# Optimization experiments

Measured on AMD Instinct MI355X. Metric: run time of the kernel, lower is better.

The kernel has to match this reference:

```python
import jax, jax.numpy as jnp
import numpy as np

NUM_CLUSTERS = 56
HEIGHT = 224
WIDTH = 224
BATCH = 32
FEAT_C = 64


def setup_inputs() -> dict:
    key = jax.random.key(0)
    combined_features = jax.random.normal(key, (BATCH, FEAT_C + 1, HEIGHT, WIDTH), dtype=jnp.float32)
    # std parameter init: num_clusters / sqrt(H*W)
    std = jnp.asarray(NUM_CLUSTERS / (HEIGHT * WIDTH) ** 0.5, dtype=jnp.float32)
    return {"combined_features": combined_features, "std": std}


def _sobel(edges):
    # edges: [B,1,H,W], 3x3 sobel with padding=1 (fixed, non-learnable filters)
    kx = jnp.array([[-1., 0., 1.], [-2., 0., 2.], [-1., 0., 1.]], jnp.float32)[None, None]
    ky = jnp.array([[-1., -2., -1.], [0., 0., 0.], [1., 2., 1.]], jnp.float32)[None, None]
    conv = lambda k: jax.lax.conv_general_dilated(edges, k, (1, 1), [(1, 1), (1, 1)])
    return conv(kx), conv(ky)


def reference(combined_features, std):
    B, Cp1, H, W = combined_features.shape
    K = NUM_CLUSTERS
    edges = combined_features[:, -1:]      # [B,1,H,W]
    features = combined_features[:, :-1]   # [B,C,H,W]

    # --- centroid seeding from edge map ---
    Gx, Gy = _sobel(edges)
    grad_mag = jnp.sqrt(Gx ** 2 + Gy ** 2)
    inverted = 1.0 - 0.5 * grad_mag                      # [B,1,H,W]
    # adaptive_avg_pool2d to (K,K); H,W divisible by K -> exact reshape-mean
    pooled = inverted[:, 0].reshape(B, K, H // K, K, W // K).mean(axis=(2, 4))  # [B,K,K]
    flat = pooled.reshape(B, K * K)
    _, idx = jax.lax.top_k(flat, K)                      # [B,K]
    sy = (idx // K).astype(jnp.float32) / K              # [B,K] in [0,1)
    sx = (idx % K).astype(jnp.float32) / K

    # --- spatial gaussian distance: separable over y and x ---
    y = (jnp.arange(H, dtype=jnp.float32) / H)[None, None, :, None]  # [1,1,H,1]
    x = (jnp.arange(W, dtype=jnp.float32) / W)[None, None, None, :]  # [1,1,1,W]
    dy = y - sy[:, :, None, None]                        # [B,K,H,1]
    dx = x - sx[:, :, None, None]                        # [B,K,1,W]
    # gauss2d(a,b,std) = (exp(-(a/std)^2) + exp(-(b/std)^2)) / 2
    spatial = (jnp.exp(-(dy / std) ** 2) + jnp.exp(-(dx / std) ** 2)) * 0.5  # [B,K,H,W]

    # --- feature distance of each pixel to global mean feature (eps=1e-6 as in F.pairwise_distance) ---
    centroid = features.mean(axis=(2, 3))                # [B,C]
    fdist = jnp.sqrt(jnp.sum((features - centroid[:, :, None, None] + 1e-6) ** 2, axis=1))  # [B,H,W]

    combined = spatial + fdist[:, None]                  # [B,K,H,W]
    markers = jax.nn.softmax(combined, axis=1)           # softmax over clusters
    return markers
```

## Files before the change

kernel.cpp:

```cpp
#include <hip/hip_runtime.h>
#include <math.h>

#define NCLUS 56
#define HH 224
#define WW 224
#define BB 32
#define CELLS (NCLUS * NCLUS)
#define HW (HH * WW)

typedef float f32x4 __attribute__((ext_vector_type(4)));

__global__ __launch_bounds__(256) void pool_kernel(const float* __restrict__ cf,
                                                   float* __restrict__ pooled) {
    __shared__ float lds[18][226];
    int b = blockIdx.x / 14;
    int grp = blockIdx.x - b * 14;
    int tid = threadIdx.x;
    const float* e = cf + ((size_t)b * 65 + 64) * HW;

    int y0 = grp * 16 - 1;
    for (int t = tid; t < 18 * 224; t += 256) {
        int r = t / 224;
        int c = t - r * 224;
        int y = y0 + r;
        lds[r][c + 1] = (y >= 0 && y < HH) ? e[y * WW + c] : 0.0f;
    }
    if (tid < 18) { lds[tid][0] = 0.0f; lds[tid][225] = 0.0f; }
    __syncthreads();

    if (tid >= 224) return;
    int lby = tid / 56;
    int bx = tid - lby * 56;
    int r0 = lby * 4;
    int c0 = bx * 4;

    float patch[6][6];
#pragma unroll
    for (int i = 0; i < 6; ++i)
#pragma unroll
        for (int j = 0; j < 6; ++j) patch[i][j] = lds[r0 + i][c0 + j];

    float s = 0.0f;
#pragma unroll
    for (int iy = 0; iy < 4; ++iy) {
#pragma unroll
        for (int ix = 0; ix < 4; ++ix) {
            float gx = (patch[iy][ix + 2] - patch[iy][ix])
                     + 2.0f * (patch[iy + 1][ix + 2] - patch[iy + 1][ix])
                     + (patch[iy + 2][ix + 2] - patch[iy + 2][ix]);
            float gy = (patch[iy + 2][ix] - patch[iy][ix])
                     + 2.0f * (patch[iy + 2][ix + 1] - patch[iy][ix + 1])
                     + (patch[iy + 2][ix + 2] - patch[iy][ix + 2]);
            float gm = sqrtf(gx * gx + gy * gy);
            s += 1.0f - 0.5f * gm;
        }
    }
    pooled[b * CELLS + (grp * 4 + lby) * NCLUS + bx] = s * 0.0625f;
}

__global__ __launch_bounds__(256) void topk_tables_kernel(
        const float* __restrict__ pooled, const float* __restrict__ stdp,
        float* __restrict__ Fx, float* __restrict__ Fy) {
    int b = blockIdx.x;
    int tid = threadIdx.x;
    __shared__ unsigned long long list[CELLS];
    __shared__ float sy_s[NCLUS], sx_s[NCLUS];
    __shared__ unsigned nlist_s;
    if (tid == 0) nlist_s = 0;

    if (tid < 64) {
        unsigned hi[49];
#pragma unroll
        for (int j = 0; j < 49; ++j) {
            int i = j * 64 + tid;
            unsigned u = __float_as_uint(pooled[b * CELLS + i]);
            hi[j] = (u & 0x80000000u) ? ~u : (u | 0x80000000u);
        }
        unsigned prefix = 0;
        unsigned cnt = CELLS;
        for (int bit = 31; bit >= 0; --bit) {
            if (cnt <= 448u) break;
            unsigned cand = prefix | (1u << bit);
            unsigned c = 0;
#pragma unroll
            for (int j = 0; j < 49; ++j) c += (hi[j] >= cand) ? 1u : 0u;
#pragma unroll
            for (int off = 32; off >= 1; off >>= 1)
                c += __shfl_xor(c, off, 64);
            if (c >= (unsigned)NCLUS) { prefix = cand; cnt = c; }
        }
#pragma unroll
        for (int j = 0; j < 49; ++j) {
            if (hi[j] >= prefix) {
                unsigned pos = atomicAdd(&nlist_s, 1u);
                unsigned i = (unsigned)(j * 64 + tid);
                list[pos] = ((unsigned long long)hi[j] << 32) |
                            (unsigned long long)(0xFFFFFFFFu - i);
            }
        }
    }
    __syncthreads();

    int N = (int)nlist_s;
    for (int c = tid; c < N; c += 256) {
        unsigned long long key = list[c];
        int r = 0;
        for (int j = 0; j < N; ++j) r += (list[j] > key) ? 1 : 0;
        if (r < NCLUS) {
            unsigned idx = 0xFFFFFFFFu - (unsigned)(key & 0xFFFFFFFFull);
            sy_s[r] = (float)(idx / NCLUS) / (float)NCLUS;
            sx_s[r] = (float)(idx % NCLUS) / (float)NCLUS;
        }
    }
    __syncthreads();

    float inv_std = 1.0f / stdp[0];
    for (int t = tid; t < NCLUS * WW; t += 256) {
        int k = t / WW;
        int w = t - k * WW;
        float tx = ((float)w / 224.0f - sx_s[k]) * inv_std;
        Fx[(size_t)b * NCLUS * WW + t] = expf(0.5f * expf(-(tx * tx)));
    }
    for (int t = tid; t < HH * NCLUS; t += 256) {
        int h = t / NCLUS;
        int k = t - h * NCLUS;
        float ty = ((float)h / 224.0f - sy_s[k]) * inv_std;
        Fy[(size_t)b * HH * NCLUS + t] = expf(0.5f * expf(-(ty * ty)));
    }
}

__global__ __launch_bounds__(448) void markers_kernel(
        const float* __restrict__ Fx, const float* __restrict__ Fy,
        float* __restrict__ out) {
    __shared__ float fx_lds[NCLUS][WW];
    __shared__ float fy_s[14 * NCLUS];
    int blk = blockIdx.x;
    int b = blk / 16;
    int h0 = (blk - b * 16) * 14;
    int tid = threadIdx.x;

    const f32x4* fxg = (const f32x4*)(Fx + (size_t)b * NCLUS * WW);
    f32x4* fxl = (f32x4*)&fx_lds[0][0];
    for (int t = tid; t < NCLUS * WW / 4; t += 448) fxl[t] = fxg[t];
    const float* fyg = Fy + ((size_t)b * HH + h0) * NCLUS;
    for (int t = tid; t < 14 * NCLUS; t += 448) fy_s[t] = fyg[t];
    __syncthreads();

#pragma unroll
    for (int q = 0; q < 2; ++q) {
        int e = q * 448 + tid;
        if (e < 14 * 56) {
            int row = e / 56;
            int wq = e - row * 56;
            const float* fyp = fy_s + row * NCLUS;

            float s0 = 0.f, s1 = 0.f, s2 = 0.f, s3 = 0.f;
#pragma unroll 8
            for (int k = 0; k < NCLUS; ++k) {
                float fy = fyp[k];
                f32x4 fx = *(const f32x4*)&fx_lds[k][wq * 4];
                s0 = fmaf(fy, fx.x, s0);
                s1 = fmaf(fy, fx.y, s1);
                s2 = fmaf(fy, fx.z, s2);
                s3 = fmaf(fy, fx.w, s3);
            }
            float r0 = 1.0f / s0, r1 = 1.0f / s1, r2 = 1.0f / s2,
                  r3 = 1.0f / s3;

            float* op = out + (size_t)b * NCLUS * HW +
                        (size_t)(h0 + row) * WW + wq * 4;
#pragma unroll 8
            for (int k = 0; k < NCLUS; ++k) {
                float fy = fyp[k];
                f32x4 fx = *(const f32x4*)&fx_lds[k][wq * 4];
                f32x4 o;
                o.x = (fy * fx.x) * r0;
                o.y = (fy * fx.y) * r1;
                o.z = (fy * fx.z) * r2;
                o.w = (fy * fx.w) * r3;
                __builtin_nontemporal_store(o, (f32x4*)op);
                op += HW;
            }
        }
    }
}

extern "C" void kernel_launch(void* const* d_in, const int* in_sizes, int n_in,
                              void* d_out, int out_size, void* d_ws,
                              size_t ws_size, hipStream_t stream) {
    const float* cf = (const float*)d_in[0];
    const float* stdp = (const float*)d_in[1];
    float* out = (float*)d_out;

    char* ws = (char*)d_ws;
    float* pooled = (float*)ws;
    float* Fx = (float*)(ws + 512 * 1024);
    float* Fy = (float*)(ws + 512 * 1024 + 2 * 1024 * 1024);

    pool_kernel<<<BB * 14, 256, 0, stream>>>(cf, pooled);
    topk_tables_kernel<<<BB, 256, 0, stream>>>(pooled, stdp, Fx, Fy);
    markers_kernel<<<512, 448, 0, stream>>>(Fx, Fy, out);
}
```

Measured before the change: 113.9 us.

## Read Fx table directly from global/L2 instead of staging in LDS, smaller row tiles

```diff
diff --git a/kernel.cpp b/kernel.cpp
--- a/kernel.cpp
+++ b/kernel.cpp
@@ -129,59 +129,47 @@
     }
 }
 
-__global__ __launch_bounds__(448) void markers_kernel(
+__global__ __launch_bounds__(448, 7) void markers_kernel(
         const float* __restrict__ Fx, const float* __restrict__ Fy,
         float* __restrict__ out) {
-    __shared__ float fx_lds[NCLUS][WW];
-    __shared__ float fy_s[14 * NCLUS];
+    __shared__ float fy_s[8 * NCLUS];
     int blk = blockIdx.x;
-    int b = blk / 16;
-    int h0 = (blk - b * 16) * 14;
+    int b = blk / 28;
+    int h0 = (blk - b * 28) * 8;
     int tid = threadIdx.x;
 
-    const f32x4* fxg = (const f32x4*)(Fx + (size_t)b * NCLUS * WW);
-    f32x4* fxl = (f32x4*)&fx_lds[0][0];
-    for (int t = tid; t < NCLUS * WW / 4; t += 448) fxl[t] = fxg[t];
-    const float* fyg = Fy + ((size_t)b * HH + h0) * NCLUS;
-    for (int t = tid; t < 14 * NCLUS; t += 448) fy_s[t] = fyg[t];
+    fy_s[tid] = Fy[((size_t)b * HH + h0) * NCLUS + tid];
     __syncthreads();
 
-#pragma unroll
-    for (int q = 0; q < 2; ++q) {
-        int e = q * 448 + tid;
-        if (e < 14 * 56) {
-            int row = e / 56;
-            int wq = e - row * 56;
-            const float* fyp = fy_s + row * NCLUS;
+    int row = tid / 56;
+    int wq = tid - row * 56;
+    const float* fyp = fy_s + row * NCLUS;
+    const f32x4* fxp = (const f32x4*)(Fx + (size_t)b * NCLUS * WW) + wq;
 
-            float s0 = 0.f, s1 = 0.f, s2 = 0.f, s3 = 0.f;
+    float s0 = 0.f, s1 = 0.f, s2 = 0.f, s3 = 0.f;
 #pragma unroll 8
-            for (int k = 0; k < NCLUS; ++k) {
-                float fy = fyp[k];
-                f32x4 fx = *(const f32x4*)&fx_lds[k][wq * 4];
-                s0 = fmaf(fy, fx.x, s0);
-                s1 = fmaf(fy, fx.y, s1);
-                s2 = fmaf(fy, fx.z, s2);
-                s3 = fmaf(fy, fx.w, s3);
-            }
-            float r0 = 1.0f / s0, r1 = 1.0f / s1, r2 = 1.0f / s2,
-                  r3 = 1.0f / s3;
+    for (int k = 0; k < NCLUS; ++k) {
+        float fy = fyp[k];
+        f32x4 fx = fxp[(size_t)k * 56];
+        s0 = fmaf(fy, fx.x, s0);
+        s1 = fmaf(fy, fx.y, s1);
+        s2 = fmaf(fy, fx.z, s2);
+        s3 = fmaf(fy, fx.w, s3);
+    }
+    float r0 = 1.0f / s0, r1 = 1.0f / s1, r2 = 1.0f / s2, r3 = 1.0f / s3;
 
-            float* op = out + (size_t)b * NCLUS * HW +
-                        (size_t)(h0 + row) * WW + wq * 4;
+    float* op = out + (size_t)b * NCLUS * HW + (size_t)(h0 + row) * WW + wq * 4;
 #pragma unroll 8
-            for (int k = 0; k < NCLUS; ++k) {
-                float fy = fyp[k];
-                f32x4 fx = *(const f32x4*)&fx_lds[k][wq * 4];
-                f32x4 o;
-                o.x = (fy * fx.x) * r0;
-                o.y = (fy * fx.y) * r1;
-                o.z = (fy * fx.z) * r2;
-                o.w = (fy * fx.w) * r3;
-                __builtin_nontemporal_store(o, (f32x4*)op);
-                op += HW;
-            }
-        }
+    for (int k = 0; k < NCLUS; ++k) {
+        float fy = fyp[k];
+        f32x4 fx = fxp[(size_t)k * 56];
+        f32x4 o;
+        o.x = (fy * fx.x) * r0;
+        o.y = (fy * fx.y) * r1;
+        o.z = (fy * fx.z) * r2;
+        o.w = (fy * fx.w) * r3;
+        __builtin_nontemporal_store(o, (f32x4*)op);
+        op += HW;
     }
 }
 
@@ -199,5 +187,5 @@
 
     pool_kernel<<<BB * 14, 256, 0, stream>>>(cf, pooled);
     topk_tables_kernel<<<BB, 256, 0, stream>>>(pooled, stdp, Fx, Fy);
-    markers_kernel<<<512, 448, 0, stream>>>(Fx, Fy, out);
+    markers_kernel<<<BB * 28, 448, 0, stream>>>(Fx, Fy, out);
 }
```

Result: no change. 113.0 us (-0.8%).
